# Kernel optimization log

Hardware: AMD Instinct MI355X
Metric: run time of the kernel (lower is better)

The kernel has to match this reference:

```python
import jax, jax.numpy as jnp
import numpy as np

N = 100000      # nodes
E = 1600000     # edges (avg degree 16)
D_IN = 128      # input feature dim
H = 128         # sage_hidden (conv1 and conv2 out)
LH = 256        # linear_hidden (decoder)


def setup_inputs() -> dict:
    key = jax.random.key(0)
    ks = jax.random.split(key, 12)
    x = jax.random.normal(ks[0], (N, D_IN), dtype=jnp.float32)
    edge_index = jax.random.randint(ks[1], (2, E), 0, N, dtype=jnp.int64)
    s = 1.0 / np.sqrt(D_IN)
    sh = 1.0 / np.sqrt(H)
    sl = 1.0 / np.sqrt(LH)
    return {
        "x": x,
        "edge_index": edge_index,
        # SAGEConv1: out = agg @ W_l^T + b_l + x @ W_r^T
        "W1_l": jax.random.uniform(ks[2], (H, D_IN), jnp.float32, -s, s),
        "b1": jax.random.uniform(ks[3], (H,), jnp.float32, -s, s),
        "W1_r": jax.random.uniform(ks[4], (H, D_IN), jnp.float32, -s, s),
        # SAGEConv2
        "W2_l": jax.random.uniform(ks[5], (H, H), jnp.float32, -sh, sh),
        "b2": jax.random.uniform(ks[6], (H,), jnp.float32, -sh, sh),
        "W2_r": jax.random.uniform(ks[7], (H, H), jnp.float32, -sh, sh),
        # decoder MLP
        "W3": jax.random.uniform(ks[8], (LH, H), jnp.float32, -sh, sh),
        "b3": jax.random.uniform(ks[9], (LH,), jnp.float32, -sh, sh),
        "W4": jax.random.uniform(ks[10], (1, LH), jnp.float32, -sl, sl),
        "b4": jax.random.uniform(ks[11], (1,), jnp.float32, -sl, sl),
    }


def _mean_aggregate(x, src, dst):
    # gather neighbor features along edges and mean-reduce into destination nodes
    sums = jax.ops.segment_sum(x[src], dst, num_segments=N)          # [N, d]
    cnt = jax.ops.segment_sum(jnp.ones((src.shape[0],), x.dtype), dst,
                              num_segments=N)                        # [N]
    return sums / jnp.maximum(cnt, 1.0)[:, None]


def _sage(x, src, dst, W_l, b, W_r):
    agg = _mean_aggregate(x, src, dst)
    return agg @ W_l.T + b + x @ W_r.T


def reference(x, edge_index, W1_l, b1, W1_r, W2_l, b2, W2_r, W3, b3, W4, b4):
    src, dst = edge_index[0], edge_index[1]
    h = jax.nn.relu(_sage(x, src, dst, W1_l, b1, W1_r))   # conv1 + relu
    h = _sage(h, src, dst, W2_l, b2, W2_r)                 # conv2
    # decoder (dropout p=0 / eval mode -> identity)
    h = jax.nn.relu(h @ W3.T + b3)
    out = (h @ W4.T + b4).reshape(-1)                      # [N]
    return out
```

## Files before the change

kernel.cpp:

```cpp
#include <hip/hip_runtime.h>

typedef unsigned short u16;
typedef unsigned int u32;
typedef unsigned long long u64;

#define N_NODES 100000
#define N_EDGES 1600000
#define TPITCH 136
#define NBIN 196
#define BCAP 12288
#define NPART 512
#define EPB 3125

typedef __bf16 bf16x8 __attribute__((ext_vector_type(8)));
typedef float  f32x4  __attribute__((ext_vector_type(4)));

__device__ inline float b2f(u16 b) { return __uint_as_float(((u32)b) << 16); }
__device__ inline float b2f_lo(u32 u) { return __uint_as_float(u << 16); }
__device__ inline float b2f_hi(u32 u) { return __uint_as_float(u & 0xffff0000u); }
__device__ inline u16 f2b(float f) {
    u32 u = __float_as_uint(f);
    return (u16)((u + 0x7fffu + ((u >> 16) & 1u)) >> 16);
}

__device__ inline bf16x8 ldfrag(const u16* base, int row, int k) {
    union { uint4 u; bf16x8 v; } t;
    t.u = *(const uint4*)(base + (size_t)row * 128 + k);
    return t.v;
}
__device__ inline bf16x8 ldfrag_f32(const float* base, int row, int k) {
    const float4* p = (const float4*)(base + (size_t)row * 128 + k);
    float4 a = p[0], b = p[1];
    union { u16 h[8]; bf16x8 v; } t;
    t.h[0] = f2b(a.x); t.h[1] = f2b(a.y); t.h[2] = f2b(a.z); t.h[3] = f2b(a.w);
    t.h[4] = f2b(b.x); t.h[5] = f2b(b.y); t.h[6] = f2b(b.z); t.h[7] = f2b(b.w);
    return t.v;
}
__device__ inline bf16x8 ldfrag_lds(const u16* tile, int lrow, int k) {
    union { uint4 u; bf16x8 v; } t;
    t.u = *(const uint4*)(tile + lrow * TPITCH + k);
    return t.v;
}
__device__ inline f32x4 mfma16(bf16x8 a, bf16x8 b, f32x4 c) {
    return __builtin_amdgcn_mfma_f32_16x16x32_bf16(a, b, c, 0, 0, 0);
}

__device__ inline void stage_w(const u16* __restrict__ g, u16* lds) {
    int t = threadIdx.x;
#pragma unroll
    for (int i = 0; i < 8; i++) {
        int u = t + i * 256;
        int row = u >> 4, k = (u & 15) * 8;
        *(uint4*)(lds + row * TPITCH + k) = *(const uint4*)(g + row * 128 + k);
    }
}

__global__ __launch_bounds__(256) void k_diag(u16* __restrict__ out, float val) {
    int i = blockIdx.x * 256 + threadIdx.x;
    if (i < N_NODES) out[i] = f2b(val);
}

__global__ __launch_bounds__(256) void k_detects(const u64* __restrict__ e,
                                                 const u32* __restrict__ x,
                                                 int* __restrict__ flags) {
    int t = threadIdx.x;
    if (blockIdx.x == 0) {
        u64 v = 0;
#pragma unroll
        for (int i = 0; i < 4; i++) v |= e[t + 256 * i];
        if (v >> 32) atomicOr(&flags[0], 1);
    } else {
        int bad = 0;
#pragma unroll
        for (int i = 0; i < 4; i++) {
            u32 w = x[t + 256 * i];
            u32 ex = (w >> 7) & 0xff;
            if (ex < 100 || ex > 140) bad = 1;
        }
        if (bad) atomicOr(&flags[1], 1);
    }
}

__device__ inline void load_edge(const int* ei, int is32, int e, int& src, int& dst) {
    if (is32) {
        src = ei[e]; dst = ei[N_EDGES + e];
    } else {
        const long long* e64 = (const long long*)ei;
        src = (int)e64[e]; dst = (int)e64[N_EDGES + e];
    }
}

__global__ __launch_bounds__(256) void k_rhist(const int* __restrict__ ei,
                                               int* __restrict__ ghist,
                                               const int* __restrict__ flags) {
    __shared__ int hist[NBIN];
    int p = blockIdx.x, t = threadIdx.x;
    for (int i = t; i < NBIN; i += 256) hist[i] = 0;
    __syncthreads();
    int is32 = flags[0];
    int base = p * EPB;
    int end = base + EPB; if (end > N_EDGES) end = N_EDGES;
    for (int e = base + t; e < end; e += 256) {
        int src, dst; load_edge(ei, is32, e, src, dst);
        if ((u32)src < N_NODES && (u32)dst < N_NODES) atomicAdd(&hist[dst >> 9], 1);
    }
    __syncthreads();
    for (int i = t; i < NBIN; i += 256) ghist[i * NPART + p] = hist[i];
}
__global__ __launch_bounds__(512) void k_rscan(const int* __restrict__ ghist,
                                               int* __restrict__ gbase,
                                               int* __restrict__ gcur) {
    __shared__ int buf[NPART];
    int b = blockIdx.x, t = threadIdx.x;
    int v = ghist[b * NPART + t];
    buf[t] = v;
    __syncthreads();
    for (int s = 1; s < NPART; s <<= 1) {
        int a = (t >= s) ? buf[t - s] : 0;
        __syncthreads();
        buf[t] += a;
        __syncthreads();
    }
    gbase[b * NPART + t] = buf[t] - v;
    if (t == NPART - 1) gcur[b] = buf[t];
}
__global__ __launch_bounds__(256) void k_rscatter(const int* __restrict__ ei,
                                                  const int* __restrict__ gbase,
                                                  u32* __restrict__ gbuf,
                                                  const int* __restrict__ flags) {
    __shared__ int cur[NBIN];
    int p = blockIdx.x, t = threadIdx.x;
    for (int i = t; i < NBIN; i += 256) cur[i] = gbase[i * NPART + p];
    __syncthreads();
    int is32 = flags[0];
    int base = p * EPB;
    int end = base + EPB; if (end > N_EDGES) end = N_EDGES;
    for (int e = base + t; e < end; e += 256) {
        int src, dst; load_edge(ei, is32, e, src, dst);
        if ((u32)src < N_NODES && (u32)dst < N_NODES) {
            int bin = dst >> 9;
            int pos = atomicAdd(&cur[bin], 1);
            if (pos < BCAP)
                gbuf[(size_t)bin * BCAP + pos] = ((u32)(dst & 511) << 17) | (u32)src;
        }
    }
}
__global__ __launch_bounds__(512) void k_binB(const int* __restrict__ gcur,
                                              const u32* __restrict__ gbuf,
                                              u32* __restrict__ csr,
                                              int* __restrict__ cnt,
                                              int* __restrict__ offN) {
    __shared__ int hist[512];
    __shared__ int pfx[512];
    __shared__ int cur[512];
    __shared__ u32 srcbuf[BCAP];
    int b = blockIdx.x, t = threadIdx.x;
    int n = gcur[b]; if (n > BCAP) n = BCAP;
    hist[t] = 0;
    __syncthreads();
    for (int i = t; i < n; i += 512)
        atomicAdd(&hist[gbuf[(size_t)b * BCAP + i] >> 17], 1);
    __syncthreads();
    pfx[t] = hist[t];
    __syncthreads();
    for (int s = 1; s < 512; s <<= 1) {
        int a = (t >= s) ? pfx[t - s] : 0;
        __syncthreads();
        pfx[t] += a;
        __syncthreads();
    }
    int excl = pfx[t] - hist[t];
    cur[t] = excl;
    __syncthreads();
    for (int i = t; i < n; i += 512) {
        u32 p = gbuf[(size_t)b * BCAP + i];
        int pos = atomicAdd(&cur[p >> 17], 1);
        if (pos < BCAP) srcbuf[pos] = p & 0x1FFFFu;
    }
    __syncthreads();
    int total = pfx[511];
    for (int i = t; i < total; i += 512)
        csr[(size_t)b * BCAP + i] = srcbuf[i];
    int node = b * 512 + t;
    if (node < N_NODES) {
        cnt[node] = hist[t];
        offN[node] = b * BCAP + excl;
    }
}

#define WTOT 99073
struct CvtArgs { const void* src[10]; int off[10]; int n[10]; };
__global__ __launch_bounds__(256) void k_cvtw(CvtArgs a, u16* __restrict__ dst,
                                              const int* __restrict__ flags) {
    int i = blockIdx.x * 256 + threadIdx.x;
    if (i >= WTOT) return;
    int isf = flags[1];
    int s = 0;
    while (s < 9 && i >= a.off[s + 1]) s++;
    int j = i - a.off[s];
    float v = isf ? ((const float*)a.src[s])[j] : b2f(((const u16*)a.src[s])[j]);
    dst[i] = f2b(v);
}
#define W_W1L 0
#define W_W1R 16384
#define W_W2L 32768
#define W_W2R 49152
#define W_W3  65536
#define W_W4  98304
#define W_B1  98560
#define W_B2  98688
#define W_B3  98816
#define W_B4  99072

__global__ __launch_bounds__(256) void k_cvtx(const void* __restrict__ x,
                                              u16* __restrict__ xb,
                                              const int* __restrict__ flags) {
    int i = blockIdx.x * 256 + threadIdx.x;
    if ((size_t)i * 4 >= (size_t)N_NODES * 128) return;
    if (flags[1]) {
        float4 v = ((const float4*)x)[i];
        union { u16 h[4]; u64 q; } t;
        t.h[0] = f2b(v.x); t.h[1] = f2b(v.y); t.h[2] = f2b(v.z); t.h[3] = f2b(v.w);
        ((u64*)xb)[i] = t.q;
    } else {
        ((u64*)xb)[i] = ((const u64*)x)[i];
    }
}

__global__ __launch_bounds__(256) void k_aggc(const u16* __restrict__ feat,
                                              const int* __restrict__ cnt,
                                              const int* __restrict__ offN,
                                              const u32* __restrict__ csr,
                                              u16* __restrict__ outb) {
    int node = blockIdx.x * 4 + (threadIdx.x >> 6);
    if (node >= N_NODES) return;
    int lane = threadIdx.x & 63;
    int deg = cnt[node];
    int s = offN[node];
    const u32* f = (const u32*)feat;
    float a0 = 0, a1 = 0, b0 = 0, b1 = 0, c0 = 0, c1 = 0, d0 = 0, d1 = 0;
    float e0 = 0, e1 = 0, g0 = 0, g1 = 0, h0f = 0, h1f = 0, i0 = 0, i1 = 0;
    int p = 0;
    for (; p + 7 < deg; p += 8) {
        u32 n0 = csr[s + p],     n1 = csr[s + p + 1], n2 = csr[s + p + 2], n3 = csr[s + p + 3];
        u32 n4 = csr[s + p + 4], n5 = csr[s + p + 5], n6 = csr[s + p + 6], n7 = csr[s + p + 7];
        if (n0 >= N_NODES) n0 = 0;
        if (n1 >= N_NODES) n1 = 0;
        if (n2 >= N_NODES) n2 = 0;
        if (n3 >= N_NODES) n3 = 0;
        if (n4 >= N_NODES) n4 = 0;
        if (n5 >= N_NODES) n5 = 0;
        if (n6 >= N_NODES) n6 = 0;
        if (n7 >= N_NODES) n7 = 0;
        u32 w0 = f[(size_t)n0 * 64 + lane];
        u32 w1 = f[(size_t)n1 * 64 + lane];
        u32 w2 = f[(size_t)n2 * 64 + lane];
        u32 w3 = f[(size_t)n3 * 64 + lane];
        u32 w4 = f[(size_t)n4 * 64 + lane];
        u32 w5 = f[(size_t)n5 * 64 + lane];
        u32 w6 = f[(size_t)n6 * 64 + lane];
        u32 w7 = f[(size_t)n7 * 64 + lane];
        a0 += b2f_lo(w0); a1 += b2f_hi(w0);
        b0 += b2f_lo(w1); b1 += b2f_hi(w1);
        c0 += b2f_lo(w2); c1 += b2f_hi(w2);
        d0 += b2f_lo(w3); d1 += b2f_hi(w3);
        e0 += b2f_lo(w4); e1 += b2f_hi(w4);
        g0 += b2f_lo(w5); g1 += b2f_hi(w5);
        h0f += b2f_lo(w6); h1f += b2f_hi(w6);
        i0 += b2f_lo(w7); i1 += b2f_hi(w7);
    }
    for (; p + 3 < deg; p += 4) {
        u32 n0 = csr[s + p], n1 = csr[s + p + 1], n2 = csr[s + p + 2], n3 = csr[s + p + 3];
        if (n0 >= N_NODES) n0 = 0;
        if (n1 >= N_NODES) n1 = 0;
        if (n2 >= N_NODES) n2 = 0;
        if (n3 >= N_NODES) n3 = 0;
        u32 w0 = f[(size_t)n0 * 64 + lane];
        u32 w1 = f[(size_t)n1 * 64 + lane];
        u32 w2 = f[(size_t)n2 * 64 + lane];
        u32 w3 = f[(size_t)n3 * 64 + lane];
        a0 += b2f_lo(w0); a1 += b2f_hi(w0);
        b0 += b2f_lo(w1); b1 += b2f_hi(w1);
        c0 += b2f_lo(w2); c1 += b2f_hi(w2);
        d0 += b2f_lo(w3); d1 += b2f_hi(w3);
    }
    for (; p < deg; p++) {
        u32 n0 = csr[s + p];
        if (n0 >= N_NODES) n0 = 0;
        u32 w0 = f[(size_t)n0 * 64 + lane];
        a0 += b2f_lo(w0); a1 += b2f_hi(w0);
    }
    float s0 = ((a0 + b0) + (c0 + d0)) + ((e0 + g0) + (h0f + i0));
    float s1 = ((a1 + b1) + (c1 + d1)) + ((e1 + g1) + (h1f + i1));
    float sc = deg > 0 ? 1.f / (float)deg : 0.f;
    u16 o0 = f2b(s0 * sc), o1 = f2b(s1 * sc);
    ((u32*)outb)[(size_t)node * 64 + lane] = (u32)o0 | ((u32)o1 << 16);
}

__global__ __launch_bounds__(256) void k_aggcx(const void* __restrict__ x,
                                               const int* __restrict__ cnt,
                                               const int* __restrict__ offN,
                                               const u32* __restrict__ csr,
                                               const int* __restrict__ flags,
                                               u16* __restrict__ outb) {
    int node = blockIdx.x * 4 + (threadIdx.x >> 6);
    if (node >= N_NODES) return;
    int lane = threadIdx.x & 63;
    int deg = cnt[node];
    int s = offN[node];
    float a0 = 0, a1 = 0, b0 = 0, b1 = 0;
    int p = 0;
    if (flags[1]) {
        const float2* f = (const float2*)x;
        for (; p + 1 < deg; p += 2) {
            u32 n0 = csr[s + p], n1 = csr[s + p + 1];
            if (n0 >= N_NODES) n0 = 0;
            if (n1 >= N_NODES) n1 = 0;
            float2 w0 = f[(size_t)n0 * 64 + lane];
            float2 w1 = f[(size_t)n1 * 64 + lane];
            a0 += w0.x; a1 += w0.y; b0 += w1.x; b1 += w1.y;
        }
        for (; p < deg; p++) {
            u32 n0 = csr[s + p];
            if (n0 >= N_NODES) n0 = 0;
            float2 w0 = f[(size_t)n0 * 64 + lane];
            a0 += w0.x; a1 += w0.y;
        }
    } else {
        const u32* f = (const u32*)x;
        for (; p + 1 < deg; p += 2) {
            u32 n0 = csr[s + p], n1 = csr[s + p + 1];
            if (n0 >= N_NODES) n0 = 0;
            if (n1 >= N_NODES) n1 = 0;
            u32 w0 = f[(size_t)n0 * 64 + lane];
            u32 w1 = f[(size_t)n1 * 64 + lane];
            a0 += b2f_lo(w0); a1 += b2f_hi(w0);
            b0 += b2f_lo(w1); b1 += b2f_hi(w1);
        }
        for (; p < deg; p++) {
            u32 n0 = csr[s + p];
            if (n0 >= N_NODES) n0 = 0;
            u32 w0 = f[(size_t)n0 * 64 + lane];
            a0 += b2f_lo(w0); a1 += b2f_hi(w0);
        }
    }
    float s0 = a0 + b0, s1 = a1 + b1;
    float sc = deg > 0 ? 1.f / (float)deg : 0.f;
    u16 o0 = f2b(s0 * sc), o1 = f2b(s1 * sc);
    ((u32*)outb)[(size_t)node * 64 + lane] = (u32)o0 | ((u32)o1 << 16);
}

template <bool DUALX>
__global__ __launch_bounds__(256) void k_conv1f(
    const u16* __restrict__ aggA, const void* __restrict__ xself,
    const u16* __restrict__ Wc, const int* __restrict__ flags,
    u16* __restrict__ h1) {
    __shared__ __align__(16) u16 wbuf[128 * TPITCH];
    int wid = threadIdx.x >> 6, lane = threadIdx.x & 63;
    int r15 = lane & 15, quad = lane >> 4;
    int rb = blockIdx.x * 64;
    int ar = rb + wid * 16 + r15; if (ar > N_NODES - 1) ar = N_NODES - 1;

    bf16x8 ag[4], ax[4];
    bool isf = DUALX && flags[1];
#pragma unroll
    for (int ks = 0; ks < 4; ks++) {
        int ko = ks * 32 + quad * 8;
        ag[ks] = ldfrag(aggA, ar, ko);
        ax[ks] = isf ? ldfrag_f32((const float*)xself, ar, ko)
                     : ldfrag((const u16*)xself, ar, ko);
    }
    f32x4 acc[8] = {};
    stage_w(Wc + W_W1L, wbuf);
    __syncthreads();
#pragma unroll
    for (int ks = 0; ks < 4; ks++) {
        int ko = ks * 32 + quad * 8;
#pragma unroll
        for (int ct = 0; ct < 8; ct++)
            acc[ct] = mfma16(ag[ks], ldfrag_lds(wbuf, ct * 16 + r15, ko), acc[ct]);
    }
    __syncthreads();
    stage_w(Wc + W_W1R, wbuf);
    __syncthreads();
#pragma unroll
    for (int ks = 0; ks < 4; ks++) {
        int ko = ks * 32 + quad * 8;
#pragma unroll
        for (int ct = 0; ct < 8; ct++)
            acc[ct] = mfma16(ax[ks], ldfrag_lds(wbuf, ct * 16 + r15, ko), acc[ct]);
    }
#pragma unroll
    for (int ct = 0; ct < 8; ct++) {
        int col = ct * 16 + r15;
        float bb = b2f(Wc[W_B1 + col]);
#pragma unroll
        for (int r = 0; r < 4; r++) {
            int row = rb + wid * 16 + quad * 4 + r;
            if (row < N_NODES)
                h1[(size_t)row * 128 + col] = f2b(fmaxf(acc[ct][r] + bb, 0.f));
        }
    }
}

__global__ __launch_bounds__(256) void k_conv2f(
    const u16* __restrict__ aggH, const u16* __restrict__ h1,
    const u16* __restrict__ Wc, const int* __restrict__ flags,
    void* __restrict__ out) {
    __shared__ __align__(16) u16 wbuf[128 * TPITCH];
    __shared__ __align__(16) u16 tile[64 * TPITCH];
    int wid = threadIdx.x >> 6, lane = threadIdx.x & 63;
    int r15 = lane & 15, quad = lane >> 4;
    int rb = blockIdx.x * 64;
    int ar = rb + wid * 16 + r15; if (ar > N_NODES - 1) ar = N_NODES - 1;
    int arl = wid * 16 + r15;

    bf16x8 at[4], as[4];
#pragma unroll
    for (int ks = 0; ks < 4; ks++) {
        int ko = ks * 32 + quad * 8;
        at[ks] = ldfrag(aggH, ar, ko);
        as[ks] = ldfrag(h1, ar, ko);
    }
    f32x4 acc2[8] = {};
    stage_w(Wc + W_W2L, wbuf);
    __syncthreads();
#pragma unroll
    for (int ks = 0; ks < 4; ks++) {
        int ko = ks * 32 + quad * 8;
#pragma unroll
        for (int ct = 0; ct < 8; ct++)
            acc2[ct] = mfma16(at[ks], ldfrag_lds(wbuf, ct * 16 + r15, ko), acc2[ct]);
    }
    __syncthreads();
    stage_w(Wc + W_W2R, wbuf);
    __syncthreads();
#pragma unroll
    for (int ks = 0; ks < 4; ks++) {
        int ko = ks * 32 + quad * 8;
#pragma unroll
        for (int ct = 0; ct < 8; ct++)
            acc2[ct] = mfma16(as[ks], ldfrag_lds(wbuf, ct * 16 + r15, ko), acc2[ct]);
    }
#pragma unroll
    for (int ct = 0; ct < 8; ct++) {
        int col = ct * 16 + r15;
        float bb = b2f(Wc[W_B2 + col]);
#pragma unroll
        for (int r = 0; r < 4; r++) {
            int lr = wid * 16 + quad * 4 + r;
            tile[lr * TPITCH + col] = f2b(acc2[ct][r] + bb);
        }
    }
    __syncthreads();

    float pr[4] = {};
    float b4f = b2f(Wc[W_B4]);
#pragma unroll
    for (int half = 0; half < 2; half++) {
        stage_w(Wc + W_W3 + half * 16384, wbuf);
        __syncthreads();
        f32x4 acc3[8] = {};
#pragma unroll
        for (int ks = 0; ks < 4; ks++) {
            int ko = ks * 32 + quad * 8;
            bf16x8 a = ldfrag_lds(tile, arl, ko);
#pragma unroll
            for (int ct = 0; ct < 8; ct++)
                acc3[ct] = mfma16(a, ldfrag_lds(wbuf, ct * 16 + r15, ko), acc3[ct]);
        }
#pragma unroll
        for (int ct = 0; ct < 8; ct++) {
            int col = half * 128 + ct * 16 + r15;
            float bb = b2f(Wc[W_B3 + col]);
            float w4 = b2f(Wc[W_W4 + col]);
#pragma unroll
            for (int r = 0; r < 4; r++)
                pr[r] += fmaxf(acc3[ct][r] + bb, 0.f) * w4;
        }
        __syncthreads();
    }
#pragma unroll
    for (int m = 1; m < 16; m <<= 1)
#pragma unroll
        for (int r = 0; r < 4; r++)
            pr[r] += __shfl_xor(pr[r], m, 64);
    if (r15 == 0) {
        int isf = flags[1];
#pragma unroll
        for (int r = 0; r < 4; r++) {
            int row = rb + wid * 16 + quad * 4 + r;
            if (row < N_NODES) {
                float v = pr[r] + b4f;
                if (isf) ((float*)out)[row] = v;
                else     ((u16*)out)[row] = f2b(v);
            }
        }
    }
}

__global__ __launch_bounds__(256) void k_hist(const int* __restrict__ ei,
                                              int* __restrict__ cnt,
                                              const int* __restrict__ flags) {
    int e = blockIdx.x * 256 + threadIdx.x;
    if (e >= N_EDGES) return;
    int src, dst; load_edge(ei, flags[0], e, src, dst);
    if ((u32)src < N_NODES && (u32)dst < N_NODES) atomicAdd(&cnt[dst], 1);
}
__global__ __launch_bounds__(1024) void k_scan(int* __restrict__ cnt,
                                               int* __restrict__ off) {
    __shared__ int buf[1024];
    __shared__ int carry_s;
    int t = threadIdx.x;
    if (t == 0) carry_s = 0;
    __syncthreads();
    for (int base = 0; base < N_NODES; base += 1024) {
        int i = base + t;
        int v = (i < N_NODES) ? cnt[i] : 0;
        buf[t] = v;
        __syncthreads();
        for (int s = 1; s < 1024; s <<= 1) {
            int a = (t >= s) ? buf[t - s] : 0;
            __syncthreads();
            buf[t] += a;
            __syncthreads();
        }
        int carry = carry_s;
        if (i < N_NODES) {
            int excl = carry + buf[t] - v;
            off[i] = excl;
            cnt[i] = excl;
        }
        __syncthreads();
        if (t == 1023) carry_s = carry + buf[1023];
        __syncthreads();
    }
    if (t == 0) off[N_NODES] = carry_s;
}
__global__ __launch_bounds__(256) void k_csr(const int* __restrict__ ei,
                                             int* __restrict__ cursor,
                                             int* __restrict__ csr,
                                             const int* __restrict__ flags) {
    int e = blockIdx.x * 256 + threadIdx.x;
    if (e >= N_EDGES) return;
    int src, dst; load_edge(ei, flags[0], e, src, dst);
    if ((u32)src < N_NODES && (u32)dst < N_NODES) {
        int pos = atomicAdd(&cursor[dst], 1);
        if ((u32)pos < N_EDGES) csr[pos] = src;
    }
}
__device__ inline void agg_bf16(const u16* __restrict__ feat,
                                const int* __restrict__ off, const int* __restrict__ csr,
                                u16* tile, int rb, int wid, int lane) {
    const u32* f32p = (const u32*)feat;
    for (int rr = 0; rr < 32; rr++) {
        int lr = wid * 32 + rr;
        int node = rb + lr;
        float s0 = 0.f, s1 = 0.f;
        int deg = 0;
        if (node < N_NODES) {
            int s = off[node], e = off[node + 1];
            if (s < 0) s = 0;
            if (e > N_EDGES) e = N_EDGES;
            if (e < s) e = s;
            deg = e - s;
            for (int p = s; p < e; p++) {
                int nb = csr[p];
                if ((u32)nb >= N_NODES) nb = 0;
                u32 u = f32p[(size_t)nb * 64 + lane];
                s0 += b2f_lo(u); s1 += b2f_hi(u);
            }
        }
        float sc = deg > 0 ? 1.f / (float)deg : 0.f;
        u16 h0 = f2b(s0 * sc), h1 = f2b(s1 * sc);
        ((u32*)tile)[lr * (TPITCH / 2) + lane] = (u32)h0 | ((u32)h1 << 16);
    }
}
__device__ inline void agg_f32(const float* __restrict__ feat,
                               const int* __restrict__ off, const int* __restrict__ csr,
                               u16* tile, int rb, int wid, int lane) {
    const float2* fp = (const float2*)feat;
    for (int rr = 0; rr < 32; rr++) {
        int lr = wid * 32 + rr;
        int node = rb + lr;
        float s0 = 0.f, s1 = 0.f;
        int deg = 0;
        if (node < N_NODES) {
            int s = off[node], e = off[node + 1];
            if (s < 0) s = 0;
            if (e > N_EDGES) e = N_EDGES;
            if (e < s) e = s;
            deg = e - s;
            for (int p = s; p < e; p++) {
                int nb = csr[p];
                if ((u32)nb >= N_NODES) nb = 0;
                float2 v = fp[(size_t)nb * 64 + lane];
                s0 += v.x; s1 += v.y;
            }
        }
        float sc = deg > 0 ? 1.f / (float)deg : 0.f;
        u16 h0 = f2b(s0 * sc), h1 = f2b(s1 * sc);
        ((u32*)tile)[lr * (TPITCH / 2) + lane] = (u32)h0 | ((u32)h1 << 16);
    }
}
__global__ __launch_bounds__(256) void k_conv1(
    const void* __restrict__ x, const int* __restrict__ off, const int* __restrict__ csr,
    const u16* __restrict__ Wc, const int* __restrict__ flags,
    u16* __restrict__ h1) {
    __shared__ __align__(16) u16 tile[128 * TPITCH];
    int wid = threadIdx.x >> 6, lane = threadIdx.x & 63;
    int r15 = lane & 15, quad = lane >> 4;
    int rb = blockIdx.x * 128;
    int isf = flags[1];
    if (isf) agg_f32((const float*)x, off, csr, tile, rb, wid, lane);
    else     agg_bf16((const u16*)x, off, csr, tile, rb, wid, lane);
    __syncthreads();
    int ar0l = wid * 32 + r15, ar1l = ar0l + 16;
    int ar0g = rb + ar0l; if (ar0g > N_NODES - 1) ar0g = N_NODES - 1;
    int ar1g = rb + ar1l; if (ar1g > N_NODES - 1) ar1g = N_NODES - 1;
    bf16x8 ax0[4], ax1[4];
    if (isf) {
#pragma unroll
        for (int ks = 0; ks < 4; ks++) {
            int ko = ks * 32 + quad * 8;
            ax0[ks] = ldfrag_f32((const float*)x, ar0g, ko);
            ax1[ks] = ldfrag_f32((const float*)x, ar1g, ko);
        }
    } else {
#pragma unroll
        for (int ks = 0; ks < 4; ks++) {
            int ko = ks * 32 + quad * 8;
            ax0[ks] = ldfrag((const u16*)x, ar0g, ko);
            ax1[ks] = ldfrag((const u16*)x, ar1g, ko);
        }
    }
    f32x4 acc[2][8] = {};
#pragma unroll
    for (int ks = 0; ks < 4; ks++) {
        int ko = ks * 32 + quad * 8;
        bf16x8 a0t = ldfrag_lds(tile, ar0l, ko);
        bf16x8 a1t = ldfrag_lds(tile, ar1l, ko);
#pragma unroll
        for (int ct = 0; ct < 8; ct++) {
            bf16x8 bl = ldfrag(Wc + W_W1L, ct * 16 + r15, ko);
            bf16x8 br = ldfrag(Wc + W_W1R, ct * 16 + r15, ko);
            acc[0][ct] = mfma16(a0t, bl, acc[0][ct]);
            acc[0][ct] = mfma16(ax0[ks], br, acc[0][ct]);
            acc[1][ct] = mfma16(a1t, bl, acc[1][ct]);
            acc[1][ct] = mfma16(ax1[ks], br, acc[1][ct]);
        }
    }
#pragma unroll
    for (int ct = 0; ct < 8; ct++) {
        int col = ct * 16 + r15;
        float bb = b2f(Wc[W_B1 + col]);
#pragma unroll
        for (int rt = 0; rt < 2; rt++) {
#pragma unroll
            for (int r = 0; r < 4; r++) {
                int row = rb + wid * 32 + rt * 16 + quad * 4 + r;
                if (row < N_NODES)
                    h1[(size_t)row * 128 + col] = f2b(fmaxf(acc[rt][ct][r] + bb, 0.f));
            }
        }
    }
}
__global__ __launch_bounds__(256) void k_conv2mlp(
    const u16* __restrict__ h1, const int* __restrict__ off, const int* __restrict__ csr,
    const u16* __restrict__ Wc, const int* __restrict__ flags,
    void* __restrict__ out) {
    __shared__ __align__(16) u16 tile[128 * TPITCH];
    int wid = threadIdx.x >> 6, lane = threadIdx.x & 63;
    int r15 = lane & 15, quad = lane >> 4;
    int rb = blockIdx.x * 128;
    agg_bf16(h1, off, csr, tile, rb, wid, lane);
    __syncthreads();
    int ar0l = wid * 32 + r15, ar1l = ar0l + 16;
    int ar0g = rb + ar0l; if (ar0g > N_NODES - 1) ar0g = N_NODES - 1;
    int ar1g = rb + ar1l; if (ar1g > N_NODES - 1) ar1g = N_NODES - 1;
    f32x4 acc2[2][8] = {};
#pragma unroll
    for (int ks = 0; ks < 4; ks++) {
        int ko = ks * 32 + quad * 8;
        bf16x8 a0t = ldfrag_lds(tile, ar0l, ko);
        bf16x8 a1t = ldfrag_lds(tile, ar1l, ko);
        bf16x8 a0s = ldfrag(h1, ar0g, ko);
        bf16x8 a1s = ldfrag(h1, ar1g, ko);
#pragma unroll
        for (int ct = 0; ct < 8; ct++) {
            bf16x8 bl = ldfrag(Wc + W_W2L, ct * 16 + r15, ko);
            bf16x8 br = ldfrag(Wc + W_W2R, ct * 16 + r15, ko);
            acc2[0][ct] = mfma16(a0t, bl, acc2[0][ct]);
            acc2[0][ct] = mfma16(a0s, br, acc2[0][ct]);
            acc2[1][ct] = mfma16(a1t, bl, acc2[1][ct]);
            acc2[1][ct] = mfma16(a1s, br, acc2[1][ct]);
        }
    }
    __syncthreads();
#pragma unroll
    for (int ct = 0; ct < 8; ct++) {
        int col = ct * 16 + r15;
        float bb = b2f(Wc[W_B2 + col]);
#pragma unroll
        for (int rt = 0; rt < 2; rt++) {
#pragma unroll
            for (int r = 0; r < 4; r++) {
                int lr = wid * 32 + rt * 16 + quad * 4 + r;
                tile[lr * TPITCH + col] = f2b(acc2[rt][ct][r] + bb);
            }
        }
    }
    __syncthreads();
    float pr[2][4] = {};
    float b4f = b2f(Wc[W_B4]);
#pragma unroll
    for (int half = 0; half < 2; half++) {
        f32x4 acc3[2][8] = {};
#pragma unroll
        for (int ks = 0; ks < 4; ks++) {
            int ko = ks * 32 + quad * 8;
            bf16x8 a0 = ldfrag_lds(tile, ar0l, ko);
            bf16x8 a1 = ldfrag_lds(tile, ar1l, ko);
#pragma unroll
            for (int ct = 0; ct < 8; ct++) {
                bf16x8 b = ldfrag(Wc + W_W3, half * 128 + ct * 16 + r15, ko);
                acc3[0][ct] = mfma16(a0, b, acc3[0][ct]);
                acc3[1][ct] = mfma16(a1, b, acc3[1][ct]);
            }
        }
#pragma unroll
        for (int ct = 0; ct < 8; ct++) {
            int col = half * 128 + ct * 16 + r15;
            float bb = b2f(Wc[W_B3 + col]);
            float w4 = b2f(Wc[W_W4 + col]);
#pragma unroll
            for (int rt = 0; rt < 2; rt++)
#pragma unroll
                for (int r = 0; r < 4; r++)
                    pr[rt][r] += fmaxf(acc3[rt][ct][r] + bb, 0.f) * w4;
        }
    }
#pragma unroll
    for (int m = 1; m < 16; m <<= 1)
#pragma unroll
        for (int rt = 0; rt < 2; rt++)
#pragma unroll
            for (int r = 0; r < 4; r++)
                pr[rt][r] += __shfl_xor(pr[rt][r], m, 64);
    if (r15 == 0) {
        int isf = flags[1];
#pragma unroll
        for (int rt = 0; rt < 2; rt++) {
#pragma unroll
            for (int r = 0; r < 4; r++) {
                int row = rb + wid * 32 + rt * 16 + quad * 4 + r;
                if (row < N_NODES) {
                    float v = pr[rt][r] + b4f;
                    if (isf) ((float*)out)[row] = v;
                    else     ((u16*)out)[row] = f2b(v);
                }
            }
        }
    }
}

extern "C" void kernel_launch(void* const* d_in, const int* in_sizes, int n_in,
                              void* d_out, int out_size, void* d_ws, size_t ws_size,
                              hipStream_t stream) {
    const void* x  = d_in[0];
    const int* ei  = (const int*)d_in[1];

    const size_t A = 256;
    const size_t sFlg  = 256;
    const size_t sGcur = 1024;
    const size_t sGh   = (((size_t)NBIN * NPART * 4) + A - 1) & ~(A - 1);
    const size_t sCnt  = (((size_t)N_NODES * 4) + A - 1) & ~(A - 1);
    const size_t sOffN = (((size_t)N_NODES * 4) + A - 1) & ~(A - 1);
    const size_t sWc   = ((WTOT * 2) + A - 1) & ~(A - 1);
    const size_t sCsrB = (((size_t)NBIN * BCAP * 4) + A - 1) & ~(A - 1);
    const size_t sFB   = (((size_t)N_NODES * 128 * 2) + A - 1) & ~(A - 1);
    const size_t sOff  = (((size_t)(N_NODES + 1) * 4) + A - 1) & ~(A - 1);
    const size_t sCsr  = (((size_t)N_EDGES * 4) + A - 1) & ~(A - 1);
    const size_t needB1 = sFlg + sGcur + 2 * sGh + sCnt + sOffN + sWc + sCsrB + 2 * sFB;
    const size_t needB0 = needB1 + sFB;
    const size_t needS  = sFlg + sCnt + sOff + sCsr + sFB;

    char* ws = (char*)d_ws;
    int gconv = (N_NODES + 63) / 64;
    int gagg  = (N_NODES + 3) / 4;

    CvtArgs ca;
    const int srcIdx[10] = {2, 4, 5, 7, 8, 10, 3, 6, 9, 11};
    const int offs[10] = {W_W1L, W_W1R, W_W2L, W_W2R, W_W3, W_W4, W_B1, W_B2, W_B3, W_B4};
    const int ns[10]   = {16384, 16384, 16384, 16384, 32768, 256, 128, 128, 256, 1};
    for (int i = 0; i < 10; i++) { ca.src[i] = d_in[srcIdx[i]]; ca.off[i] = offs[i]; ca.n[i] = ns[i]; }

    if (ws_size >= needB1) {
        bool t0 = ws_size >= needB0;
        int* flags = (int*)ws;
        int* gcur  = (int*)(ws + sFlg);
        int* ghist = (int*)(ws + sFlg + sGcur);
        int* gbase = (int*)(ws + sFlg + sGcur + sGh);
        int* cnt   = (int*)(ws + sFlg + sGcur + 2 * sGh);
        int* offN  = (int*)(ws + sFlg + sGcur + 2 * sGh + sCnt);
        u16* Wc    = (u16*)(ws + sFlg + sGcur + 2 * sGh + sCnt + sOffN);
        u32* csrb  = (u32*)(ws + sFlg + sGcur + 2 * sGh + sCnt + sOffN + sWc);
        u16* B1    = (u16*)(ws + sFlg + sGcur + 2 * sGh + sCnt + sOffN + sWc + sCsrB);
        u16* B2    = B1 + (sFB / 2);
        u32* gbuf  = (u32*)B2;
        u16* xb    = B2 + (sFB / 2);

        hipMemsetAsync(ws, 0, sFlg, stream);
        k_detects<<<2, 256, 0, stream>>>((const u64*)ei, (const u32*)x, flags);
        k_rhist<<<NPART, 256, 0, stream>>>(ei, ghist, flags);
        k_rscan<<<NBIN, 512, 0, stream>>>(ghist, gbase, gcur);
        k_rscatter<<<NPART, 256, 0, stream>>>(ei, gbase, gbuf, flags);
        k_binB<<<NBIN, 512, 0, stream>>>(gcur, gbuf, csrb, cnt, offN);
        k_cvtw<<<(WTOT + 255) / 256, 256, 0, stream>>>(ca, Wc, flags);

        if (t0) {
            k_cvtx<<<((N_NODES * 128 / 4) + 255) / 256, 256, 0, stream>>>(x, xb, flags);
            k_aggc<<<gagg, 256, 0, stream>>>(xb, cnt, offN, csrb, B1);
            k_conv1f<false><<<gconv, 256, 0, stream>>>(B1, xb, Wc, flags, B2);
        } else {
            k_aggcx<<<gagg, 256, 0, stream>>>(x, cnt, offN, csrb, flags, B1);
            k_conv1f<true><<<gconv, 256, 0, stream>>>(B1, x, Wc, flags, B2);
        }
        k_aggc<<<gagg, 256, 0, stream>>>(B2, cnt, offN, csrb, B1);
        k_conv2f<<<gconv, 256, 0, stream>>>(B1, B2, Wc, flags, d_out);
    } else if (ws_size >= needS) {
        int* flags = (int*)ws;
        int* cnt   = (int*)(ws + sFlg);
        u16* Wc    = (u16*)(ws + sFlg);
        int* off   = (int*)(ws + sFlg + sCnt);
        int* csr   = (int*)(ws + sFlg + sCnt + sOff);
        u16* h1    = (u16*)(ws + sFlg + sCnt + sOff + sCsr);

        hipMemsetAsync(ws, 0, sFlg + (size_t)N_NODES * 4, stream);
        k_detects<<<2, 256, 0, stream>>>((const u64*)ei, (const u32*)x, flags);
        k_hist<<<N_EDGES / 256, 256, 0, stream>>>(ei, cnt, flags);
        k_scan<<<1, 1024, 0, stream>>>(cnt, off);
        k_csr<<<N_EDGES / 256, 256, 0, stream>>>(ei, cnt, csr, flags);
        k_cvtw<<<(WTOT + 255) / 256, 256, 0, stream>>>(ca, Wc, flags);
        k_conv1<<<(N_NODES + 127) / 128, 256, 0, stream>>>(x, off, csr, Wc, flags, h1);
        k_conv2mlp<<<(N_NODES + 127) / 128, 256, 0, stream>>>(h1, off, csr, Wc, flags, d_out);
    } else {
        k_diag<<<(N_NODES + 255) / 256, 256, 0, stream>>>(
            (u16*)d_out, 2000.0f + (float)(ws_size >> 20));
    }
}
```

Before: 330.5 us.

## Fuse neighbor aggregation into conv GEMM kernels via LDS tile

Factors the per-node mean aggregation into a device helper and adds fused kernels that aggregate 64 nodes into shared memory and then run the SAGE MFMA GEMMs (plus the decoder MLP for layer 2) from that tile. This drops the round trip of the aggregated features through global memory and two kernel launches on the t0 path. The trade-off is that each wave now aggregates 16 nodes serially before any compute, and the larger fused kernels may lose latency hiding or occupancy compared with the separate, wide aggregation kernels.

After: 502.3 us. 52.0% more time.

```diff
diff --git a/kernel.cpp b/kernel.cpp
--- a/kernel.cpp
+++ b/kernel.cpp
@@ -227,16 +227,9 @@
     }
 }
 
-__global__ __launch_bounds__(256) void k_aggc(const u16* __restrict__ feat,
-                                              const int* __restrict__ cnt,
-                                              const int* __restrict__ offN,
-                                              const u32* __restrict__ csr,
-                                              u16* __restrict__ outb) {
-    int node = blockIdx.x * 4 + (threadIdx.x >> 6);
-    if (node >= N_NODES) return;
-    int lane = threadIdx.x & 63;
-    int deg = cnt[node];
-    int s = offN[node];
+__device__ inline u32 agg_node_pack(const u16* __restrict__ feat,
+                                    const u32* __restrict__ csr,
+                                    int s, int deg, int lane) {
     const u32* f = (const u32*)feat;
     float a0 = 0, a1 = 0, b0 = 0, b1 = 0, c0 = 0, c1 = 0, d0 = 0, d1 = 0;
     float e0 = 0, e1 = 0, g0 = 0, g1 = 0, h0f = 0, h1f = 0, i0 = 0, i1 = 0;
@@ -294,7 +287,19 @@
     float s1 = ((a1 + b1) + (c1 + d1)) + ((e1 + g1) + (h1f + i1));
     float sc = deg > 0 ? 1.f / (float)deg : 0.f;
     u16 o0 = f2b(s0 * sc), o1 = f2b(s1 * sc);
-    ((u32*)outb)[(size_t)node * 64 + lane] = (u32)o0 | ((u32)o1 << 16);
+    return (u32)o0 | ((u32)o1 << 16);
+}
+
+__global__ __launch_bounds__(256) void k_aggc(const u16* __restrict__ feat,
+                                              const int* __restrict__ cnt,
+                                              const int* __restrict__ offN,
+                                              const u32* __restrict__ csr,
+                                              u16* __restrict__ outb) {
+    int node = blockIdx.x * 4 + (threadIdx.x >> 6);
+    if (node >= N_NODES) return;
+    int lane = threadIdx.x & 63;
+    u32 pk = agg_node_pack(feat, csr, offN[node], cnt[node], lane);
+    ((u32*)outb)[(size_t)node * 64 + lane] = pk;
 }
 
 __global__ __launch_bounds__(256) void k_aggcx(const void* __restrict__ x,
@@ -350,6 +355,134 @@
     ((u32*)outb)[(size_t)node * 64 + lane] = (u32)o0 | ((u32)o1 << 16);
 }
 
+__global__ __launch_bounds__(256) void k_fc1(
+    const u16* __restrict__ xb, const int* __restrict__ cnt,
+    const int* __restrict__ offN, const u32* __restrict__ csr,
+    const u16* __restrict__ Wc, u16* __restrict__ h1) {
+    __shared__ __align__(16) u16 tile[64 * TPITCH];
+    int wid = threadIdx.x >> 6, lane = threadIdx.x & 63;
+    int r15 = lane & 15, quad = lane >> 4;
+    int rb = blockIdx.x * 64;
+    for (int i = 0; i < 16; i++) {
+        int node = rb + wid * 16 + i;
+        if (node > N_NODES - 1) node = N_NODES - 1;
+        u32 pk = agg_node_pack(xb, csr, offN[node], cnt[node], lane);
+        ((u32*)tile)[(wid * 16 + i) * (TPITCH / 2) + lane] = pk;
+    }
+    int ar = rb + wid * 16 + r15; if (ar > N_NODES - 1) ar = N_NODES - 1;
+    int arl = wid * 16 + r15;
+    f32x4 acc[8] = {};
+#pragma unroll
+    for (int ks = 0; ks < 4; ks++) {
+        int ko = ks * 32 + quad * 8;
+        bf16x8 ag = ldfrag_lds(tile, arl, ko);
+        bf16x8 ax = ldfrag(xb, ar, ko);
+#pragma unroll
+        for (int ct = 0; ct < 8; ct++) {
+            bf16x8 bl = ldfrag(Wc + W_W1L, ct * 16 + r15, ko);
+            bf16x8 br = ldfrag(Wc + W_W1R, ct * 16 + r15, ko);
+            acc[ct] = mfma16(ag, bl, acc[ct]);
+            acc[ct] = mfma16(ax, br, acc[ct]);
+        }
+    }
+#pragma unroll
+    for (int ct = 0; ct < 8; ct++) {
+        int col = ct * 16 + r15;
+        float bb = b2f(Wc[W_B1 + col]);
+#pragma unroll
+        for (int r = 0; r < 4; r++) {
+            int row = rb + wid * 16 + quad * 4 + r;
+            if (row < N_NODES)
+                h1[(size_t)row * 128 + col] = f2b(fmaxf(acc[ct][r] + bb, 0.f));
+        }
+    }
+}
+
+__global__ __launch_bounds__(256) void k_fc2(
+    const u16* __restrict__ h1, const int* __restrict__ cnt,
+    const int* __restrict__ offN, const u32* __restrict__ csr,
+    const u16* __restrict__ Wc, const int* __restrict__ flags,
+    void* __restrict__ out) {
+    __shared__ __align__(16) u16 tile[64 * TPITCH];
+    int wid = threadIdx.x >> 6, lane = threadIdx.x & 63;
+    int r15 = lane & 15, quad = lane >> 4;
+    int rb = blockIdx.x * 64;
+    for (int i = 0; i < 16; i++) {
+        int node = rb + wid * 16 + i;
+        if (node > N_NODES - 1) node = N_NODES - 1;
+        u32 pk = agg_node_pack(h1, csr, offN[node], cnt[node], lane);
+        ((u32*)tile)[(wid * 16 + i) * (TPITCH / 2) + lane] = pk;
+    }
+    int ar = rb + wid * 16 + r15; if (ar > N_NODES - 1) ar = N_NODES - 1;
+    int arl = wid * 16 + r15;
+    f32x4 acc2[8] = {};
+#pragma unroll
+    for (int ks = 0; ks < 4; ks++) {
+        int ko = ks * 32 + quad * 8;
+        bf16x8 at = ldfrag_lds(tile, arl, ko);
+        bf16x8 as = ldfrag(h1, ar, ko);
+#pragma unroll
+        for (int ct = 0; ct < 8; ct++) {
+            bf16x8 bl = ldfrag(Wc + W_W2L, ct * 16 + r15, ko);
+            bf16x8 br = ldfrag(Wc + W_W2R, ct * 16 + r15, ko);
+            acc2[ct] = mfma16(at, bl, acc2[ct]);
+            acc2[ct] = mfma16(as, br, acc2[ct]);
+        }
+    }
+#pragma unroll
+    for (int ct = 0; ct < 8; ct++) {
+        int col = ct * 16 + r15;
+        float bb = b2f(Wc[W_B2 + col]);
+#pragma unroll
+        for (int r = 0; r < 4; r++) {
+            int lr = wid * 16 + quad * 4 + r;
+            tile[lr * TPITCH + col] = f2b(acc2[ct][r] + bb);
+        }
+    }
+    float pr[4] = {};
+    float b4f = b2f(Wc[W_B4]);
+#pragma unroll
+    for (int half = 0; half < 2; half++) {
+        f32x4 acc3[8] = {};
+#pragma unroll
+        for (int ks = 0; ks < 4; ks++) {
+            int ko = ks * 32 + quad * 8;
+            bf16x8 a = ldfrag_lds(tile, arl, ko);
+#pragma unroll
+            for (int ct = 0; ct < 8; ct++) {
+                bf16x8 b = ldfrag(Wc + W_W3, half * 128 + ct * 16 + r15, ko);
+                acc3[ct] = mfma16(a, b, acc3[ct]);
+            }
+        }
+#pragma unroll
+        for (int ct = 0; ct < 8; ct++) {
+            int col = half * 128 + ct * 16 + r15;
+            float bb = b2f(Wc[W_B3 + col]);
+            float w4 = b2f(Wc[W_W4 + col]);
+#pragma unroll
+            for (int r = 0; r < 4; r++)
+                pr[r] += fmaxf(acc3[ct][r] + bb, 0.f) * w4;
+        }
+    }
+#pragma unroll
+    for (int m = 1; m < 16; m <<= 1)
+#pragma unroll
+        for (int r = 0; r < 4; r++)
+            pr[r] += __shfl_xor(pr[r], m, 64);
+    if (r15 == 0) {
+        int isf = flags[1];
+#pragma unroll
+        for (int r = 0; r < 4; r++) {
+            int row = rb + wid * 16 + quad * 4 + r;
+            if (row < N_NODES) {
+                float v = pr[r] + b4f;
+                if (isf) ((float*)out)[row] = v;
+                else     ((u16*)out)[row] = f2b(v);
+            }
+        }
+    }
+}
+
 template <bool DUALX>
 __global__ __launch_bounds__(256) void k_conv1f(
     const u16* __restrict__ aggA, const void* __restrict__ xself,
@@ -820,14 +953,14 @@
 
         if (t0) {
             k_cvtx<<<((N_NODES * 128 / 4) + 255) / 256, 256, 0, stream>>>(x, xb, flags);
-            k_aggc<<<gagg, 256, 0, stream>>>(xb, cnt, offN, csrb, B1);
-            k_conv1f<false><<<gconv, 256, 0, stream>>>(B1, xb, Wc, flags, B2);
+            k_fc1<<<gconv, 256, 0, stream>>>(xb, cnt, offN, csrb, Wc, B2);
+            k_fc2<<<gconv, 256, 0, stream>>>(B2, cnt, offN, csrb, Wc, flags, d_out);
         } else {
             k_aggcx<<<gagg, 256, 0, stream>>>(x, cnt, offN, csrb, flags, B1);
             k_conv1f<true><<<gconv, 256, 0, stream>>>(B1, x, Wc, flags, B2);
-        }
-        k_aggc<<<gagg, 256, 0, stream>>>(B2, cnt, offN, csrb, B1);
-        k_conv2f<<<gconv, 256, 0, stream>>>(B1, B2, Wc, flags, d_out);
+            k_aggc<<<gagg, 256, 0, stream>>>(B2, cnt, offN, csrb, B1);
+            k_conv2f<<<gconv, 256, 0, stream>>>(B1, B2, Wc, flags, d_out);
+        }
     } else if (ws_size >= needS) {
         int* flags = (int*)ws;
         int* cnt   = (int*)(ws + sFlg);
```
